# Kernel optimization log

Measured on AMD Instinct MI355X. Metric: run time of the kernel, lower is better.

Reference implementation:

```python
import jax, jax.numpy as jnp
import numpy as np

N = 50000
E = 600000
IN_C = 128
OUT_C = 64
HID = 2 * OUT_C  # 128


def setup_inputs() -> dict:
    key = jax.random.key(0)
    ks = jax.random.split(key, 8)
    x = jax.random.normal(ks[0], (N, IN_C), dtype=jnp.float32)
    edge_index = jax.random.randint(ks[1], (2, E), 0, N, dtype=jnp.int64)
    # Glorot-style init for GCN weights, zero bias (PyG default)
    def glorot(k, fan_in, fan_out):
        s = jnp.sqrt(6.0 / (fan_in + fan_out)).astype(jnp.float32)
        return jax.random.uniform(k, (fan_in, fan_out), jnp.float32, -s, s)
    return {
        "x": x,
        "edge_index": edge_index,
        "W1": glorot(ks[2], IN_C, HID),
        "b1": jnp.zeros((HID,), jnp.float32),
        "W_mu": glorot(ks[3], HID, OUT_C),
        "b_mu": jnp.zeros((OUT_C,), jnp.float32),
        "W_ls": glorot(ks[4], HID, OUT_C),
        "b_ls": jnp.zeros((OUT_C,), jnp.float32),
    }


def _gcn_norm(edge_index, num_nodes):
    # Add self-loops, compute symmetric normalization (cached=True in original
    # means this is computed once and reused by all three convs -- same math).
    loop = jnp.arange(num_nodes, dtype=edge_index.dtype)
    row = jnp.concatenate([edge_index[0], loop])  # source
    col = jnp.concatenate([edge_index[1], loop])  # target
    deg = jax.ops.segment_sum(jnp.ones_like(col, dtype=jnp.float32), col,
                              num_segments=num_nodes)
    dis = jnp.where(deg > 0, jax.lax.rsqrt(deg), 0.0)  # deg^{-1/2}, inf->0
    norm = dis[row] * dis[col]  # [E+N]
    return row, col, norm


def _gcn_conv(x, W, b, row, col, norm, num_nodes):
    h = x @ W                                  # dense transform [N, out]
    msg = h[row] * norm[:, None]               # gather + scale [E+N, out]
    out = jax.ops.segment_sum(msg, col, num_segments=num_nodes)
    return out + b


def reference(x, edge_index, W1, b1, W_mu, b_mu, W_ls, b_ls):
    num_nodes = x.shape[0]
    row, col, norm = _gcn_norm(edge_index, num_nodes)
    # eval mode: F.dropout is identity when not training
    h = jax.nn.relu(_gcn_conv(x, W1, b1, row, col, norm, num_nodes))
    mu = _gcn_conv(h, W_mu, b_mu, row, col, norm, num_nodes)
    logstd = _gcn_conv(h, W_ls, b_ls, row, col, norm, num_nodes)
    return mu, logstd
```

## Files before the change

### kernel.cpp

```cpp
#include <hip/hip_runtime.h>
#include <hip/hip_fp16.h>


#define N_NODES 50000
#define N_EDGES 600000
#define MU_SIZE (N_NODES * 64)
#define SCAN_BLOCKS 200
#define SCAN_CHUNK 250
#define WT_S 136

typedef _Float16 half8 __attribute__((ext_vector_type(8)));
typedef float floatx4 __attribute__((ext_vector_type(4)));

union H8 { __half2 h2[4]; float4 f4; };

__global__ __launch_bounds__(256) void count_kernel(const int* __restrict__ col,
                                                    int* __restrict__ counts, int e) {
  int i = blockIdx.x * 256 + threadIdx.x;
  if (i < e) atomicAdd(&counts[col[i]], 1);
}

__global__ __launch_bounds__(256) void blocksum_dis_kernel(const int* __restrict__ counts,
                                                           float* __restrict__ dis,
                                                           int* __restrict__ blocksums) {
  __shared__ int red[4];
  int b = blockIdx.x, t = threadIdx.x;
  int i = b * SCAN_CHUNK + t;
  int c = 0;
  if (t < SCAN_CHUNK) {
    c = counts[i];
    dis[i] = rsqrtf((float)(c + 1));
  }
  int s = c;
#pragma unroll
  for (int off = 32; off > 0; off >>= 1) s += __shfl_down(s, off, 64);
  if ((t & 63) == 0) red[t >> 6] = s;
  __syncthreads();
  if (t == 0) blocksums[b] = red[0] + red[1] + red[2] + red[3];
}

__global__ __launch_bounds__(256) void offsets_kernel(const int* __restrict__ counts,
                                                      const int* __restrict__ blocksums,
                                                      int* __restrict__ offsets) {
  __shared__ int sb[256];
  __shared__ int loc[256];
  int b = blockIdx.x, t = threadIdx.x;
  sb[t] = (t < SCAN_BLOCKS) ? blocksums[t] : 0;
  __syncthreads();
#pragma unroll
  for (int off = 1; off < 256; off <<= 1) {
    int v = (t >= off) ? sb[t - off] : 0;
    __syncthreads();
    sb[t] += v;
    __syncthreads();
  }
  int base = (b == 0) ? 0 : sb[b - 1];
  int i = b * SCAN_CHUNK + t;
  int c = (t < SCAN_CHUNK) ? counts[i] : 0;
  loc[t] = c;
  __syncthreads();
#pragma unroll
  for (int off = 1; off < 256; off <<= 1) {
    int v = (t >= off) ? loc[t - off] : 0;
    __syncthreads();
    loc[t] += v;
    __syncthreads();
  }
  if (t < SCAN_CHUNK) offsets[i] = base + loc[t] - c;
  if (b == SCAN_BLOCKS - 1 && t == SCAN_CHUNK - 1) offsets[N_NODES] = base + loc[t];
}

__global__ __launch_bounds__(256) void fill_kernel(const int* __restrict__ row,
                                                   const int* __restrict__ col,
                                                   const int* __restrict__ offsets,
                                                   int* __restrict__ fillcnt,
                                                   int* __restrict__ srcidx, int e) {
  int i = blockIdx.x * 256 + threadIdx.x;
  if (i < e) {
    int c = col[i];
    int pos = offsets[c] + atomicAdd(&fillcnt[c], 1);
    srcidx[pos] = row[i];
  }
}

template <bool SPLIT>
__global__ __launch_bounds__(256) void gemm_mfma_kernel(const float* __restrict__ X,
                                                        const _Float16* __restrict__ Xh,
                                                        const float* __restrict__ Wa,
                                                        const float* __restrict__ Wb,
                                                        const float* __restrict__ dis,
                                                        const float* __restrict__ ba,
                                                        const float* __restrict__ bb,
                                                        _Float16* __restrict__ Yh,
                                                        float* __restrict__ Yf) {
  __shared__ _Float16 WT[128 * WT_S];

  int t = threadIdx.x;
  for (int idx = t; idx < 128 * 128; idx += 256) {
    int k = idx >> 7, n = idx & 127;
    float w;
    if (!SPLIT) {
      w = Wa[k * 128 + n];
    } else {
      w = (n < 64) ? Wa[k * 64 + n] : Wb[k * 64 + (n - 64)];
    }
    WT[n * WT_S + k] = (_Float16)w;
  }
  __syncthreads();

  int wid = t >> 6, lane = t & 63;
  int q = lane >> 4, m = lane & 15;
  int r0 = blockIdx.x * 64 + wid * 16;

  size_t ar = (size_t)min(r0 + m, N_NODES - 1);
  half8 afrag[4];
  if (!SPLIT) {
#pragma unroll
    for (int c = 0; c < 4; ++c) {
      const float* ap = &X[ar * 128 + 32 * c + 8 * q];
      float4 a0 = *(const float4*)ap;
      float4 a1 = *(const float4*)(ap + 4);
      half8 af = {(_Float16)a0.x, (_Float16)a0.y, (_Float16)a0.z, (_Float16)a0.w,
                  (_Float16)a1.x, (_Float16)a1.y, (_Float16)a1.z, (_Float16)a1.w};
      afrag[c] = af;
    }
  } else {
#pragma unroll
    for (int c = 0; c < 4; ++c) {
      afrag[c] = *(const half8*)&Xh[ar * 128 + 32 * c + 8 * q];
    }
  }

  int orow[4];
  float dv[4];
#pragma unroll
  for (int g = 0; g < 4; ++g) {
    orow[g] = r0 + 4 * q + g;
    if (!SPLIT) dv[g] = dis[min(orow[g], N_NODES - 1)];
  }

#pragma unroll
  for (int n = 0; n < 8; ++n) {
    floatx4 acc = {0.f, 0.f, 0.f, 0.f};
#pragma unroll
    for (int c = 0; c < 4; ++c) {
      half8 bfrag = *(const half8*)&WT[(16 * n + m) * WT_S + 32 * c + 8 * q];
      acc = __builtin_amdgcn_mfma_f32_16x16x32_f16(afrag[c], bfrag, acc, 0, 0, 0);
    }
    int colg = 16 * n + m;
    if (!SPLIT) {
#pragma unroll
      for (int g = 0; g < 4; ++g) {
        if (orow[g] < N_NODES)
          Yh[(size_t)orow[g] * 128 + colg] = (_Float16)(acc[g] * dv[g]);
      }
    } else {
      float bias = (colg < 64) ? ba[colg] : bb[colg - 64];
      size_t obase = (colg < 64) ? (size_t)colg : (size_t)MU_SIZE + (colg - 64);
#pragma unroll
      for (int g = 0; g < 4; ++g) {
        if (orow[g] < N_NODES)
          Yf[obase + (size_t)orow[g] * 64] = acc[g] + bias;
      }
    }
  }
}

template <bool BIAS_RELU>
__global__ __launch_bounds__(256) void aggregate_kernel(const __half* __restrict__ Hs,
                                                        const int* __restrict__ offsets,
                                                        const int* __restrict__ srcidx,
                                                        const float* __restrict__ dis,
                                                        const float* __restrict__ bias,
                                                        __half* __restrict__ outH, int n) {
  int wid = threadIdx.x >> 6, lane = threadIdx.x & 63;
  int q = lane >> 4, ql = lane & 15;
  int i = blockIdx.x * 4 + wid;
  if (i >= n) return;
  float di = dis[i];
  float4 selfv = ((const float4*)(Hs + (size_t)i * 128))[ql];
  float acc[8] = {0.f, 0.f, 0.f, 0.f, 0.f, 0.f, 0.f, 0.f};
  int beg = offsets[i], end = offsets[i + 1];
  int k = beg + q;
  for (; k + 4 < end; k += 8) {
    int r0 = srcidx[k];
    int r1 = srcidx[k + 4];
    float4 v0 = ((const float4*)(Hs + (size_t)r0 * 128))[ql];
    float4 v1 = ((const float4*)(Hs + (size_t)r1 * 128))[ql];
    const __half2* a0 = (const __half2*)&v0;
    const __half2* a1 = (const __half2*)&v1;
#pragma unroll
    for (int j = 0; j < 4; ++j) {
      float2 f0 = __half22float2(a0[j]);
      float2 f1 = __half22float2(a1[j]);
      acc[2 * j] += f0.x + f1.x;
      acc[2 * j + 1] += f0.y + f1.y;
    }
  }
  if (k < end) {
    int r0 = srcidx[k];
    float4 v0 = ((const float4*)(Hs + (size_t)r0 * 128))[ql];
    const __half2* a0 = (const __half2*)&v0;
#pragma unroll
    for (int j = 0; j < 4; ++j) {
      float2 f0 = __half22float2(a0[j]);
      acc[2 * j] += f0.x;
      acc[2 * j + 1] += f0.y;
    }
  }
#pragma unroll
  for (int j = 0; j < 8; ++j) {
    acc[j] += __shfl(acc[j], lane ^ 16, 64);
    acc[j] += __shfl(acc[j], lane ^ 32, 64);
  }
  if (q == 0) {
    const __half2* sh = (const __half2*)&selfv;
    float s[8];
#pragma unroll
    for (int j = 0; j < 4; ++j) {
      float2 f = __half22float2(sh[j]);
      s[2 * j] = di * (acc[2 * j] + f.x);
      s[2 * j + 1] = di * (acc[2 * j + 1] + f.y);
    }
    H8 u;
    if (BIAS_RELU) {
      float4 b0 = ((const float4*)bias)[2 * ql];
      float4 b1 = ((const float4*)bias)[2 * ql + 1];
      u.h2[0] = __float22half2_rn(
          make_float2(di * fmaxf(s[0] + b0.x, 0.f), di * fmaxf(s[1] + b0.y, 0.f)));
      u.h2[1] = __float22half2_rn(
          make_float2(di * fmaxf(s[2] + b0.z, 0.f), di * fmaxf(s[3] + b0.w, 0.f)));
      u.h2[2] = __float22half2_rn(
          make_float2(di * fmaxf(s[4] + b1.x, 0.f), di * fmaxf(s[5] + b1.y, 0.f)));
      u.h2[3] = __float22half2_rn(
          make_float2(di * fmaxf(s[6] + b1.z, 0.f), di * fmaxf(s[7] + b1.w, 0.f)));
    } else {
      u.h2[0] = __float22half2_rn(make_float2(s[0], s[1]));
      u.h2[1] = __float22half2_rn(make_float2(s[2], s[3]));
      u.h2[2] = __float22half2_rn(make_float2(s[4], s[5]));
      u.h2[3] = __float22half2_rn(make_float2(s[6], s[7]));
    }
    ((float4*)(outH + (size_t)i * 128))[ql] = u.f4;
  }
}

extern "C" void kernel_launch(void* const* d_in, const int* in_sizes, int n_in,
                              void* d_out, int out_size, void* d_ws, size_t ws_size,
                              hipStream_t stream) {
  const float* x = (const float*)d_in[0];
  const int* ei = (const int*)d_in[1];
  const float* W1 = (const float*)d_in[2];
  const float* b1 = (const float*)d_in[3];
  const float* Wmu = (const float*)d_in[4];
  const float* bmu = (const float*)d_in[5];
  const float* Wls = (const float*)d_in[6];
  const float* bls = (const float*)d_in[7];
  float* out = (float*)d_out;

  const int* row = ei;
  const int* col = ei + N_EDGES;

  __half* bufAh = (__half*)d_ws;
  __half* bufBh = bufAh + 6400000;
  __half* bufCh = bufBh + 6400000;
  float* dis = (float*)(bufCh + 6400000);
  int* counts = (int*)(dis + N_NODES);
  int* fillcnt = counts + N_NODES;
  int* offsets = fillcnt + N_NODES;
  int* srcidx = offsets + N_NODES + 1;
  int* blocksums = srcidx + N_EDGES;

  hipMemsetAsync(counts, 0, 2 * N_NODES * sizeof(int), stream);

  int eb = (N_EDGES + 255) / 256;
  count_kernel<<<eb, 256, 0, stream>>>(col, counts, N_EDGES);
  blocksum_dis_kernel<<<SCAN_BLOCKS, 256, 0, stream>>>(counts, dis, blocksums);
  offsets_kernel<<<SCAN_BLOCKS, 256, 0, stream>>>(counts, blocksums, offsets);
  fill_kernel<<<eb, 256, 0, stream>>>(row, col, offsets, fillcnt, srcidx, N_EDGES);

  int gb = (N_NODES + 63) / 64;
  gemm_mfma_kernel<false><<<gb, 256, 0, stream>>>(x, nullptr, W1, nullptr, dis, nullptr,
                                                  nullptr, (_Float16*)bufAh, nullptr);
  aggregate_kernel<true><<<N_NODES / 4, 256, 0, stream>>>(bufAh, offsets, srcidx, dis, b1,
                                                          bufBh, N_NODES);
  aggregate_kernel<false><<<N_NODES / 4, 256, 0, stream>>>(bufBh, offsets, srcidx, dis,
                                                           nullptr, bufCh, N_NODES);
  gemm_mfma_kernel<true><<<gb, 256, 0, stream>>>(nullptr, (const _Float16*)bufCh, Wmu, Wls,
                                                 nullptr, bmu, bls, nullptr, out);
}
```

Before: 230.5 us.

## Pre-transpose weights, persistent GEMM with swapped MFMA operands, quarter-wave aggregation

Adds a prep kernel that converts and transposes the weights to fp16 once, so each GEMM block copies them into LDS with vector loads instead of converting strided floats itself. The GEMM becomes a grid-stride loop over 512 blocks and swaps the MFMA operands so each lane holds four consecutive output features, allowing vectorized half4/float4 stores. Aggregation now gives each 16-lane quarter-wave its own node with a 4-way unrolled gather, which removes the cross-quarter shuffle reduction. The cost is one extra launch and per-node load imbalance inside a wave when degrees differ.

```diff
diff --git a/kernel.cpp b/kernel.cpp
--- a/kernel.cpp
+++ b/kernel.cpp
@@ -10,6 +10,7 @@
 #define WT_S 136
 
 typedef _Float16 half8 __attribute__((ext_vector_type(8)));
+typedef _Float16 half4 __attribute__((ext_vector_type(4)));
 typedef float floatx4 __attribute__((ext_vector_type(4)));
 
 union H8 { __half2 h2[4]; float4 f4; };
@@ -83,84 +84,94 @@
   }
 }
 
+__global__ __launch_bounds__(256) void prep_wt_kernel(const float* __restrict__ W1,
+                                                      const float* __restrict__ Wmu,
+                                                      const float* __restrict__ Wls,
+                                                      _Float16* __restrict__ W1T,
+                                                      _Float16* __restrict__ W2T) {
+  int idx = blockIdx.x * 256 + threadIdx.x;
+  int e = idx & 16383;
+  int n = e >> 7, k = e & 127;
+  if (idx < 16384) {
+    W1T[e] = (_Float16)W1[k * 128 + n];
+  } else {
+    float w = (n < 64) ? Wmu[k * 64 + n] : Wls[k * 64 + (n - 64)];
+    W2T[e] = (_Float16)w;
+  }
+}
+
 template <bool SPLIT>
 __global__ __launch_bounds__(256) void gemm_mfma_kernel(const float* __restrict__ X,
                                                         const _Float16* __restrict__ Xh,
-                                                        const float* __restrict__ Wa,
-                                                        const float* __restrict__ Wb,
+                                                        const _Float16* __restrict__ WT,
                                                         const float* __restrict__ dis,
                                                         const float* __restrict__ ba,
                                                         const float* __restrict__ bb,
                                                         _Float16* __restrict__ Yh,
                                                         float* __restrict__ Yf) {
-  __shared__ _Float16 WT[128 * WT_S];
+  __shared__ _Float16 WL[128 * WT_S];
 
   int t = threadIdx.x;
-  for (int idx = t; idx < 128 * 128; idx += 256) {
-    int k = idx >> 7, n = idx & 127;
-    float w;
-    if (!SPLIT) {
-      w = Wa[k * 128 + n];
-    } else {
-      w = (n < 64) ? Wa[k * 64 + n] : Wb[k * 64 + (n - 64)];
-    }
-    WT[n * WT_S + k] = (_Float16)w;
+  for (int idx = t; idx < 128 * 16; idx += 256) {
+    int n = idx >> 4, kk = (idx & 15) * 8;
+    *(half8*)&WL[n * WT_S + kk] = *(const half8*)&WT[n * 128 + kk];
   }
   __syncthreads();
 
   int wid = t >> 6, lane = t & 63;
   int q = lane >> 4, m = lane & 15;
-  int r0 = blockIdx.x * 64 + wid * 16;
-
-  size_t ar = (size_t)min(r0 + m, N_NODES - 1);
-  half8 afrag[4];
-  if (!SPLIT) {
-#pragma unroll
-    for (int c = 0; c < 4; ++c) {
-      const float* ap = &X[ar * 128 + 32 * c + 8 * q];
-      float4 a0 = *(const float4*)ap;
-      float4 a1 = *(const float4*)(ap + 4);
-      half8 af = {(_Float16)a0.x, (_Float16)a0.y, (_Float16)a0.z, (_Float16)a0.w,
-                  (_Float16)a1.x, (_Float16)a1.y, (_Float16)a1.z, (_Float16)a1.w};
-      afrag[c] = af;
-    }
-  } else {
-#pragma unroll
-    for (int c = 0; c < 4; ++c) {
-      afrag[c] = *(const half8*)&Xh[ar * 128 + 32 * c + 8 * q];
-    }
-  }
-
-  int orow[4];
-  float dv[4];
-#pragma unroll
-  for (int g = 0; g < 4; ++g) {
-    orow[g] = r0 + 4 * q + g;
-    if (!SPLIT) dv[g] = dis[min(orow[g], N_NODES - 1)];
-  }
-
-#pragma unroll
-  for (int n = 0; n < 8; ++n) {
-    floatx4 acc = {0.f, 0.f, 0.f, 0.f};
-#pragma unroll
-    for (int c = 0; c < 4; ++c) {
-      half8 bfrag = *(const half8*)&WT[(16 * n + m) * WT_S + 32 * c + 8 * q];
-      acc = __builtin_amdgcn_mfma_f32_16x16x32_f16(afrag[c], bfrag, acc, 0, 0, 0);
-    }
-    int colg = 16 * n + m;
+  const int ngroups = (N_NODES + 63) / 64;
+
+  for (int g64 = blockIdx.x; g64 < ngroups; g64 += gridDim.x) {
+    int node = g64 * 64 + wid * 16 + m;
+    size_t nr = (size_t)min(node, N_NODES - 1);
+    bool valid = node < N_NODES;
+
+    half8 xfrag[4];
     if (!SPLIT) {
 #pragma unroll
-      for (int g = 0; g < 4; ++g) {
-        if (orow[g] < N_NODES)
-          Yh[(size_t)orow[g] * 128 + colg] = (_Float16)(acc[g] * dv[g]);
+      for (int c = 0; c < 4; ++c) {
+        const float* ap = &X[nr * 128 + 32 * c + 8 * q];
+        float4 a0 = *(const float4*)ap;
+        float4 a1 = *(const float4*)(ap + 4);
+        half8 af = {(_Float16)a0.x, (_Float16)a0.y, (_Float16)a0.z, (_Float16)a0.w,
+                    (_Float16)a1.x, (_Float16)a1.y, (_Float16)a1.z, (_Float16)a1.w};
+        xfrag[c] = af;
       }
     } else {
-      float bias = (colg < 64) ? ba[colg] : bb[colg - 64];
-      size_t obase = (colg < 64) ? (size_t)colg : (size_t)MU_SIZE + (colg - 64);
-#pragma unroll
-      for (int g = 0; g < 4; ++g) {
-        if (orow[g] < N_NODES)
-          Yf[obase + (size_t)orow[g] * 64] = acc[g] + bias;
+#pragma unroll
+      for (int c = 0; c < 4; ++c) {
+        xfrag[c] = *(const half8*)&Xh[nr * 128 + 32 * c + 8 * q];
+      }
+    }
+    float dnode = SPLIT ? 0.f : dis[nr];
+
+#pragma unroll
+    for (int f = 0; f < 8; ++f) {
+      floatx4 acc = {0.f, 0.f, 0.f, 0.f};
+#pragma unroll
+      for (int c = 0; c < 4; ++c) {
+        half8 wfrag = *(const half8*)&WL[(16 * f + m) * WT_S + 32 * c + 8 * q];
+        acc = __builtin_amdgcn_mfma_f32_16x16x32_f16(wfrag, xfrag[c], acc, 0, 0, 0);
+      }
+      int fbase = 16 * f + 4 * q;
+      if (!SPLIT) {
+        if (valid) {
+          half4 o = {(_Float16)(acc[0] * dnode), (_Float16)(acc[1] * dnode),
+                     (_Float16)(acc[2] * dnode), (_Float16)(acc[3] * dnode)};
+          *(half4*)&Yh[(size_t)node * 128 + fbase] = o;
+        }
+      } else {
+        float4 bias = (f < 4) ? *(const float4*)&ba[fbase]
+                              : *(const float4*)&bb[fbase - 64];
+        float4 o = make_float4(acc[0] + bias.x, acc[1] + bias.y, acc[2] + bias.z,
+                               acc[3] + bias.w);
+        if (valid) {
+          if (f < 4)
+            *(float4*)&Yf[(size_t)node * 64 + fbase] = o;
+          else
+            *(float4*)&Yf[MU_SIZE + (size_t)node * 64 + (fbase - 64)] = o;
+        }
       }
     }
   }
@@ -175,29 +186,36 @@
                                                         __half* __restrict__ outH, int n) {
   int wid = threadIdx.x >> 6, lane = threadIdx.x & 63;
   int q = lane >> 4, ql = lane & 15;
-  int i = blockIdx.x * 4 + wid;
+  int i = blockIdx.x * 16 + wid * 4 + q;
   if (i >= n) return;
   float di = dis[i];
   float4 selfv = ((const float4*)(Hs + (size_t)i * 128))[ql];
   float acc[8] = {0.f, 0.f, 0.f, 0.f, 0.f, 0.f, 0.f, 0.f};
-  int beg = offsets[i], end = offsets[i + 1];
-  int k = beg + q;
-  for (; k + 4 < end; k += 8) {
+  int k = offsets[i], end = offsets[i + 1];
+  for (; k + 3 < end; k += 4) {
     int r0 = srcidx[k];
-    int r1 = srcidx[k + 4];
+    int r1 = srcidx[k + 1];
+    int r2 = srcidx[k + 2];
+    int r3 = srcidx[k + 3];
     float4 v0 = ((const float4*)(Hs + (size_t)r0 * 128))[ql];
     float4 v1 = ((const float4*)(Hs + (size_t)r1 * 128))[ql];
+    float4 v2 = ((const float4*)(Hs + (size_t)r2 * 128))[ql];
+    float4 v3 = ((const float4*)(Hs + (size_t)r3 * 128))[ql];
     const __half2* a0 = (const __half2*)&v0;
     const __half2* a1 = (const __half2*)&v1;
+    const __half2* a2 = (const __half2*)&v2;
+    const __half2* a3 = (const __half2*)&v3;
 #pragma unroll
     for (int j = 0; j < 4; ++j) {
       float2 f0 = __half22float2(a0[j]);
       float2 f1 = __half22float2(a1[j]);
-      acc[2 * j] += f0.x + f1.x;
-      acc[2 * j + 1] += f0.y + f1.y;
+      float2 f2 = __half22float2(a2[j]);
+      float2 f3 = __half22float2(a3[j]);
+      acc[2 * j] += (f0.x + f1.x) + (f2.x + f3.x);
+      acc[2 * j + 1] += (f0.y + f1.y) + (f2.y + f3.y);
     }
   }
-  if (k < end) {
+  for (; k < end; ++k) {
     int r0 = srcidx[k];
     float4 v0 = ((const float4*)(Hs + (size_t)r0 * 128))[ql];
     const __half2* a0 = (const __half2*)&v0;
@@ -208,40 +226,33 @@
       acc[2 * j + 1] += f0.y;
     }
   }
-#pragma unroll
-  for (int j = 0; j < 8; ++j) {
-    acc[j] += __shfl(acc[j], lane ^ 16, 64);
-    acc[j] += __shfl(acc[j], lane ^ 32, 64);
-  }
-  if (q == 0) {
-    const __half2* sh = (const __half2*)&selfv;
-    float s[8];
-#pragma unroll
-    for (int j = 0; j < 4; ++j) {
-      float2 f = __half22float2(sh[j]);
-      s[2 * j] = di * (acc[2 * j] + f.x);
-      s[2 * j + 1] = di * (acc[2 * j + 1] + f.y);
-    }
-    H8 u;
-    if (BIAS_RELU) {
-      float4 b0 = ((const float4*)bias)[2 * ql];
-      float4 b1 = ((const float4*)bias)[2 * ql + 1];
-      u.h2[0] = __float22half2_rn(
-          make_float2(di * fmaxf(s[0] + b0.x, 0.f), di * fmaxf(s[1] + b0.y, 0.f)));
-      u.h2[1] = __float22half2_rn(
-          make_float2(di * fmaxf(s[2] + b0.z, 0.f), di * fmaxf(s[3] + b0.w, 0.f)));
-      u.h2[2] = __float22half2_rn(
-          make_float2(di * fmaxf(s[4] + b1.x, 0.f), di * fmaxf(s[5] + b1.y, 0.f)));
-      u.h2[3] = __float22half2_rn(
-          make_float2(di * fmaxf(s[6] + b1.z, 0.f), di * fmaxf(s[7] + b1.w, 0.f)));
-    } else {
-      u.h2[0] = __float22half2_rn(make_float2(s[0], s[1]));
-      u.h2[1] = __float22half2_rn(make_float2(s[2], s[3]));
-      u.h2[2] = __float22half2_rn(make_float2(s[4], s[5]));
-      u.h2[3] = __float22half2_rn(make_float2(s[6], s[7]));
-    }
-    ((float4*)(outH + (size_t)i * 128))[ql] = u.f4;
-  }
+  const __half2* sh = (const __half2*)&selfv;
+  float s[8];
+#pragma unroll
+  for (int j = 0; j < 4; ++j) {
+    float2 f = __half22float2(sh[j]);
+    s[2 * j] = di * (acc[2 * j] + f.x);
+    s[2 * j + 1] = di * (acc[2 * j + 1] + f.y);
+  }
+  H8 u;
+  if (BIAS_RELU) {
+    float4 b0 = ((const float4*)bias)[2 * ql];
+    float4 b1 = ((const float4*)bias)[2 * ql + 1];
+    u.h2[0] = __float22half2_rn(
+        make_float2(di * fmaxf(s[0] + b0.x, 0.f), di * fmaxf(s[1] + b0.y, 0.f)));
+    u.h2[1] = __float22half2_rn(
+        make_float2(di * fmaxf(s[2] + b0.z, 0.f), di * fmaxf(s[3] + b0.w, 0.f)));
+    u.h2[2] = __float22half2_rn(
+        make_float2(di * fmaxf(s[4] + b1.x, 0.f), di * fmaxf(s[5] + b1.y, 0.f)));
+    u.h2[3] = __float22half2_rn(
+        make_float2(di * fmaxf(s[6] + b1.z, 0.f), di * fmaxf(s[7] + b1.w, 0.f)));
+  } else {
+    u.h2[0] = __float22half2_rn(make_float2(s[0], s[1]));
+    u.h2[1] = __float22half2_rn(make_float2(s[2], s[3]));
+    u.h2[2] = __float22half2_rn(make_float2(s[4], s[5]));
+    u.h2[3] = __float22half2_rn(make_float2(s[6], s[7]));
+  }
+  ((float4*)(outH + (size_t)i * 128))[ql] = u.f4;
 }
 
 extern "C" void kernel_launch(void* const* d_in, const int* in_sizes, int n_in,
@@ -269,8 +280,12 @@
   int* offsets = fillcnt + N_NODES;
   int* srcidx = offsets + N_NODES + 1;
   int* blocksums = srcidx + N_EDGES;
+  _Float16* W1T = (_Float16*)(blocksums + 256);
+  _Float16* W2T = W1T + 16384;
 
   hipMemsetAsync(counts, 0, 2 * N_NODES * sizeof(int), stream);
+
+  prep_wt_kernel<<<128, 256, 0, stream>>>(W1, Wmu, Wls, W1T, W2T);
 
   int eb = (N_EDGES + 255) / 256;
   count_kernel<<<eb, 256, 0, stream>>>(col, counts, N_EDGES);
@@ -278,13 +293,13 @@
   offsets_kernel<<<SCAN_BLOCKS, 256, 0, stream>>>(counts, blocksums, offsets);
   fill_kernel<<<eb, 256, 0, stream>>>(row, col, offsets, fillcnt, srcidx, N_EDGES);
 
-  int gb = (N_NODES + 63) / 64;
-  gemm_mfma_kernel<false><<<gb, 256, 0, stream>>>(x, nullptr, W1, nullptr, dis, nullptr,
-                                                  nullptr, (_Float16*)bufAh, nullptr);
-  aggregate_kernel<true><<<N_NODES / 4, 256, 0, stream>>>(bufAh, offsets, srcidx, dis, b1,
-                                                          bufBh, N_NODES);
-  aggregate_kernel<false><<<N_NODES / 4, 256, 0, stream>>>(bufBh, offsets, srcidx, dis,
-                                                           nullptr, bufCh, N_NODES);
-  gemm_mfma_kernel<true><<<gb, 256, 0, stream>>>(nullptr, (const _Float16*)bufCh, Wmu, Wls,
-                                                 nullptr, bmu, bls, nullptr, out);
-}
+  gemm_mfma_kernel<false><<<512, 256, 0, stream>>>(x, nullptr, W1T, dis, nullptr, nullptr,
+                                                   (_Float16*)bufAh, nullptr);
+  int ab = (N_NODES + 15) / 16;
+  aggregate_kernel<true><<<ab, 256, 0, stream>>>(bufAh, offsets, srcidx, dis, b1,
+                                                 bufBh, N_NODES);
+  aggregate_kernel<false><<<ab, 256, 0, stream>>>(bufBh, offsets, srcidx, dis,
+                                                  nullptr, bufCh, N_NODES);
+  gemm_mfma_kernel<true><<<512, 256, 0, stream>>>(nullptr, (const _Float16*)bufCh, W2T,
+                                                  nullptr, bmu, bls, nullptr, out);
+}
```

Result: faster. 222.0 us, median of 2 (-3.7%).
